# Kernel tuning notes

Hardware: AMD Instinct MI355X
Metric: run time of the kernel (lower is better)

The kernel has to match this reference:

```python
import jax, jax.numpy as jnp
import numpy as np

NUM_GROUPS = 32
EPS = 1e-5


def group_norm(x, scale, bias):
    b, c, h, w = x.shape
    g = NUM_GROUPS
    xg = x.reshape(b, g, c // g, h, w)
    mean = xg.mean(axis=(2, 3, 4), keepdims=True)
    var = xg.var(axis=(2, 3, 4), keepdims=True)
    xn = (xg - mean) * jax.lax.rsqrt(var + EPS)
    xn = xn.reshape(b, c, h, w)
    return xn * scale[None, :, None, None] + bias[None, :, None, None]


def conv1x1(x, w, b):
    # x: [b,c,h,w], w: [o,c], b: [o]
    return jnp.einsum('oc,bchw->bohw', w, x) + b[None, :, None, None]


def setup_inputs() -> dict:
    key = jax.random.key(0)
    ks = jax.random.split(key, 8)
    b, c, h, w = 16, 512, 32, 32
    fan = 1.0 / np.sqrt(c)
    return {
        'x': jax.random.normal(ks[0], (b, c, h, w), dtype=jnp.float32),
        'time_emb': jax.random.normal(ks[1], (b, c), dtype=jnp.float32),
        'y': jax.random.randint(ks[2], (b,), 0, 1000, dtype=jnp.int64),
        'gn_scale': jnp.ones((c,), dtype=jnp.float32),
        'gn_bias': jnp.zeros((c,), dtype=jnp.float32),
        'w_qkv': jax.random.normal(ks[3], (3 * c, c), dtype=jnp.float32) * fan,
        'b_qkv': jax.random.normal(ks[4], (3 * c,), dtype=jnp.float32) * fan,
        'w_out': jax.random.normal(ks[5], (c, c), dtype=jnp.float32) * fan,
        'b_out': jax.random.normal(ks[6], (c,), dtype=jnp.float32) * fan,
    }


def reference(x, time_emb, y, gn_scale, gn_bias, w_qkv, b_qkv, w_out, b_out):
    b, c, h, w = x.shape
    qkv = conv1x1(group_norm(x, gn_scale, gn_bias), w_qkv, b_qkv)  # [b,3c,h,w]
    q, k, v = jnp.split(qkv, 3, axis=1)
    n = h * w
    q = q.transpose(0, 2, 3, 1).reshape(b, n, c)  # [b,n,c]
    k = k.reshape(b, c, n)                        # [b,c,n]
    v = v.transpose(0, 2, 3, 1).reshape(b, n, c)  # [b,n,c]
    scores = jnp.einsum('bnc,bcm->bnm', q, k) * (c ** -0.5)  # [b,n,n]
    attn = jax.nn.softmax(scores, axis=-1)
    out = jnp.einsum('bnm,bmc->bnc', attn, v)     # [b,n,c]
    out = out.reshape(b, h, w, c).transpose(0, 3, 1, 2)
    return conv1x1(out, w_out, b_out) + x
```

## Files before the change

kernel.cpp:

```cpp
#include <hip/hip_runtime.h>
#include <hip/hip_bf16.h>

#define NB   16
#define NC   512
#define NSPA 1024
#define NO3  1536
#define GN_EPS 1e-5f
#define SCL 0.044194173824159216f

typedef __bf16 bf16x8 __attribute__((ext_vector_type(8)));
typedef __bf16 bf16x4 __attribute__((ext_vector_type(4)));
typedef float  f32x4  __attribute__((ext_vector_type(4)));

typedef __attribute__((address_space(3))) void lds_t;
typedef const __attribute__((address_space(1))) void gl_t;
#define GLDS16(g, l) __builtin_amdgcn_global_load_lds((gl_t*)(g), (lds_t*)(l), 16, 0, 0)

__device__ __forceinline__ __bf16 tob(float f) { return (__bf16)f; }

__device__ __forceinline__ int xcd_swz(int cpx) {
  return (blockIdx.x & 7) * cpx + (blockIdx.x >> 3);
}

__global__ void gn_stats_kernel(const float* __restrict__ x,
                                const float* __restrict__ gn_scale,
                                const float* __restrict__ gn_bias,
                                float* __restrict__ coefA,
                                float* __restrict__ coefB) {
  const int L = xcd_swz(64);
  const int b = L >> 5, g = L & 31;
  const float4* base = (const float4*)(x + (size_t)(b * NC + g * 16) * NSPA);
  const int tid = threadIdx.x;
  float s = 0.f, ss = 0.f;
#pragma unroll
  for (int i = 0; i < 16; ++i) {
    float4 v = base[i * 256 + tid];
    s  += (v.x + v.y) + (v.z + v.w);
    ss += (v.x * v.x + v.y * v.y) + (v.z * v.z + v.w * v.w);
  }
#pragma unroll
  for (int off = 32; off; off >>= 1) {
    s  += __shfl_xor(s, off);
    ss += __shfl_xor(ss, off);
  }
  __shared__ float rs[4], rss[4];
  const int wave = tid >> 6, lane = tid & 63;
  if (lane == 0) { rs[wave] = s; rss[wave] = ss; }
  __syncthreads();
  if (tid < 16) {
    float S  = rs[0] + rs[1] + rs[2] + rs[3];
    float SS = rss[0] + rss[1] + rss[2] + rss[3];
    float mean = S * (1.f / 16384.f);
    float var  = SS * (1.f / 16384.f) - mean * mean;
    float rstd = rsqrtf(var + GN_EPS);
    int c = g * 16 + tid;
    float a = gn_scale[c] * rstd;
    coefA[b * NC + c] = a;
    coefB[b * NC + c] = gn_bias[c] - mean * a;
  }
}

__global__ void pack_w_kernel(const float* __restrict__ wq, const float* __restrict__ wo,
                              __bf16* __restrict__ wqb, __bf16* __restrict__ wob) {
  const int t = blockIdx.x * 256 + threadIdx.x;
  const int NQ = NO3 * NC / 4;
  float4 v;
  __bf16* dst;
  if (t < NQ) { v = ((const float4*)wq)[t]; dst = wqb + (size_t)t * 4; }
  else        { v = ((const float4*)wo)[t - NQ]; dst = wob + (size_t)(t - NQ) * 4; }
  bf16x4 w;
  w[0] = tob(v.x); w[1] = tob(v.y); w[2] = tob(v.z); w[3] = tob(v.w);
  *(bf16x4*)dst = w;
}

__global__ void pack_x_kernel(const float* __restrict__ x,
                              const float* __restrict__ coefA,
                              const float* __restrict__ coefB,
                              __bf16* __restrict__ xnT) {
  const int L = xcd_swz(256);
  const int b = L >> 7, rem = L & 127;
  const int c0 = (rem >> 4) * 64, n0 = (rem & 15) * 64;
  __shared__ __bf16 l[64][72];
  const int tid = threadIdx.x;
  const int cl = tid >> 2, seg = (tid & 3) * 16;
  const float ca = coefA[b * NC + c0 + cl], cb = coefB[b * NC + c0 + cl];
  const float4* src = (const float4*)(x + (size_t)(b * NC + c0 + cl) * NSPA + n0 + seg);
#pragma unroll
  for (int i = 0; i < 4; ++i) {
    float4 v = src[i];
    l[seg + i * 4 + 0][cl] = tob(v.x * ca + cb);
    l[seg + i * 4 + 1][cl] = tob(v.y * ca + cb);
    l[seg + i * 4 + 2][cl] = tob(v.z * ca + cb);
    l[seg + i * 4 + 3][cl] = tob(v.w * ca + cb);
  }
  __syncthreads();
#pragma unroll
  for (int i = 0; i < 2; ++i) {
    const int chunk = tid + i * 256;
    const int row = chunk >> 3, s = chunk & 7;
    *(bf16x8*)(xnT + (size_t)(b * NSPA + n0 + row) * NC + c0 + s * 8) =
        *(const bf16x8*)&l[row][s * 8];
  }
}

__device__ __forceinline__ void stage_pair(const __bf16* __restrict__ A, int lda,
                                           const __bf16* __restrict__ B, int ldb,
                                           int k0, __bf16* lAf, __bf16* lBf) {
  const int tid = threadIdx.x;
#pragma unroll
  for (int i = 0; i < 4; ++i) {
    const int idx = tid + i * 256;
    const int srow = idx >> 3;
    const int ss = ((idx & 7) ^ (srow & 7)) * 8;
    GLDS16(A + (size_t)srow * lda + k0 + ss, lAf + idx * 8);
    GLDS16(B + (size_t)srow * ldb + k0 + ss, lBf + idx * 8);
  }
}

__device__ __forceinline__ void gemm_core_db(const __bf16* __restrict__ A, int lda,
                                             const __bf16* __restrict__ B, int ldb,
                                             int K, __bf16 (*lA)[128][64],
                                             __bf16 (*lB)[128][64], f32x4 acc[4][4]) {
  const int tid = threadIdx.x;
  const int lane = tid & 63, wave = tid >> 6;
  const int wm = (wave >> 1) * 64, wn = (wave & 1) * 64;
  const int fr = lane & 15, fg = (lane >> 4) * 8;
  const int nt = K >> 6;

  stage_pair(A, lda, B, ldb, 0, &lA[0][0][0], &lB[0][0][0]);
  asm volatile("s_waitcnt vmcnt(0)" ::: "memory");
  __syncthreads();
  int cur = 0;
  for (int t = 0; t < nt; ++t) {
    if (t + 1 < nt)
      stage_pair(A, lda, B, ldb, (t + 1) * 64, &lA[cur ^ 1][0][0], &lB[cur ^ 1][0][0]);
    __builtin_amdgcn_s_setprio(1);
#pragma unroll
    for (int ks = 0; ks < 2; ++ks) {
      bf16x8 af[4], bfr[4];
#pragma unroll
      for (int mi = 0; mi < 4; ++mi) {
        const int r = wm + mi * 16 + fr;
        af[mi] = *(const bf16x8*)&lA[cur][r][(ks * 32 + fg) ^ ((r & 7) << 3)];
      }
#pragma unroll
      for (int ni = 0; ni < 4; ++ni) {
        const int r = wn + ni * 16 + fr;
        bfr[ni] = *(const bf16x8*)&lB[cur][r][(ks * 32 + fg) ^ ((r & 7) << 3)];
      }
#pragma unroll
      for (int mi = 0; mi < 4; ++mi)
#pragma unroll
        for (int ni = 0; ni < 4; ++ni)
          acc[mi][ni] = __builtin_amdgcn_mfma_f32_16x16x32_bf16(af[mi], bfr[ni], acc[mi][ni], 0, 0, 0);
    }
    __builtin_amdgcn_s_setprio(0);
    if (t + 1 < nt) {
      asm volatile("s_waitcnt vmcnt(0)" ::: "memory");
      __syncthreads();
      cur ^= 1;
    }
  }
}

__global__ __launch_bounds__(256, 2) void qkv_gemm_kernel(
    const __bf16* __restrict__ wqb, const __bf16* __restrict__ xnT,
    const float* __restrict__ bqkv, __bf16* __restrict__ qk, __bf16* __restrict__ v) {
  const int L = xcd_swz(192);
  const int pair = L / 12, mblk = L - pair * 12;
  const int b = pair >> 3;
  const int n0 = (pair & 7) * 128, m0 = mblk * 128;
  __shared__ __bf16 lA[2][128][64], lB[2][128][64];
  f32x4 acc[4][4] = {};
  gemm_core_db(wqb + (size_t)m0 * NC, NC, xnT + ((size_t)b * NSPA + n0) * NC, NC,
               NC, lA, lB, acc);

  const int lane = threadIdx.x & 63, wave = threadIdx.x >> 6;
  const int wm = (wave >> 1) * 64, wn = (wave & 1) * 64;
  const int fr = lane & 15, fq4 = (lane >> 4) * 4;
  if (m0 < NSPA) {
#pragma unroll
    for (int mi = 0; mi < 4; ++mi) {
      const int m = m0 + wm + mi * 16 + fq4;
      const float4 bias = *(const float4*)(bqkv + m);
#pragma unroll
      for (int ni = 0; ni < 4; ++ni) {
        const int n = n0 + wn + ni * 16 + fr;
        bf16x4 w;
        w[0] = tob(acc[mi][ni][0] + bias.x);
        w[1] = tob(acc[mi][ni][1] + bias.y);
        w[2] = tob(acc[mi][ni][2] + bias.z);
        w[3] = tob(acc[mi][ni][3] + bias.w);
        *(bf16x4*)(qk + ((size_t)b * NSPA + n) * NSPA + m) = w;
      }
    }
  } else {
#pragma unroll
    for (int mi = 0; mi < 4; ++mi) {
      const int m = m0 + wm + mi * 16 + fq4;
      const float4 bias = *(const float4*)(bqkv + m);
      const int vr = m - NSPA;
#pragma unroll
      for (int ni = 0; ni < 4; ++ni) {
        const int n = n0 + wn + ni * 16 + fr;
        v[((size_t)b * NC + vr + 0) * NSPA + n] = tob(acc[mi][ni][0] + bias.x);
        v[((size_t)b * NC + vr + 1) * NSPA + n] = tob(acc[mi][ni][1] + bias.y);
        v[((size_t)b * NC + vr + 2) * NSPA + n] = tob(acc[mi][ni][2] + bias.z);
        v[((size_t)b * NC + vr + 3) * NSPA + n] = tob(acc[mi][ni][3] + bias.w);
      }
    }
  }
}

__global__ __launch_bounds__(256, 2) void scores_kernel(const __bf16* __restrict__ qk,
                                                        __bf16* __restrict__ P) {
  const int L = xcd_swz(128);
  const int b = L >> 6, r = L & 63;
  const int i0 = (r >> 3) * 128, j0 = (r & 7) * 128;
  const __bf16* base = qk + (size_t)b * NSPA * NSPA;
  __shared__ __bf16 lA[2][128][64], lB[2][128][64];
  f32x4 acc[4][4] = {};
  gemm_core_db(base + (size_t)j0 * NSPA + NC, NSPA, base + (size_t)i0 * NSPA, NSPA,
               NC, lA, lB, acc);

  const int lane = threadIdx.x & 63, wave = threadIdx.x >> 6;
  const int wm = (wave >> 1) * 64, wn = (wave & 1) * 64;
  const int fr = lane & 15, fq4 = (lane >> 4) * 4;
#pragma unroll
  for (int mi = 0; mi < 4; ++mi) {
    const int j = j0 + wm + mi * 16 + fq4;
#pragma unroll
    for (int ni = 0; ni < 4; ++ni) {
      const int i = i0 + wn + ni * 16 + fr;
      bf16x4 w;
      w[0] = tob(acc[mi][ni][0] * SCL);
      w[1] = tob(acc[mi][ni][1] * SCL);
      w[2] = tob(acc[mi][ni][2] * SCL);
      w[3] = tob(acc[mi][ni][3] * SCL);
      *(bf16x4*)(P + ((size_t)b * NSPA + i) * NSPA + j) = w;
    }
  }
}

__global__ void softmax_kernel(__bf16* __restrict__ P) {
  const int L = xcd_swz(128);
  const int base_row = L * 16 + (threadIdx.x >> 6) * 4;
  const int lane = threadIdx.x & 63;
#pragma unroll
  for (int r = 0; r < 4; ++r) {
    __bf16* p = P + (size_t)(base_row + r) * NSPA + lane * 16;
    bf16x8 v0 = *(const bf16x8*)p;
    bf16x8 v1 = *(const bf16x8*)(p + 8);
    float f[16];
#pragma unroll
    for (int i = 0; i < 8; ++i) { f[i] = (float)v0[i]; f[8 + i] = (float)v1[i]; }
    float m = f[0];
#pragma unroll
    for (int i = 1; i < 16; ++i) m = fmaxf(m, f[i]);
#pragma unroll
    for (int off = 32; off; off >>= 1) m = fmaxf(m, __shfl_xor(m, off));
    float s = 0.f;
#pragma unroll
    for (int i = 0; i < 16; ++i) { f[i] = __expf(f[i] - m); s += f[i]; }
#pragma unroll
    for (int off = 32; off; off >>= 1) s += __shfl_xor(s, off);
    const float inv = 1.f / s;
#pragma unroll
    for (int i = 0; i < 8; ++i) { v0[i] = tob(f[i] * inv); v1[i] = tob(f[8 + i] * inv); }
    *(bf16x8*)p = v0;
    *(bf16x8*)(p + 8) = v1;
  }
}

__global__ __launch_bounds__(256, 2) void pv_kernel(const __bf16* __restrict__ v,
                                                    const __bf16* __restrict__ P,
                                                    __bf16* __restrict__ attn) {
  const int L = xcd_swz(64);
  const int b = L >> 5, r = L & 31;
  const int d0 = (r >> 3) * 128, i0 = (r & 7) * 128;
  __shared__ __bf16 lA[2][128][64], lB[2][128][64];
  f32x4 acc[4][4] = {};
  gemm_core_db(v + ((size_t)b * NC + d0) * NSPA, NSPA,
               P + ((size_t)b * NSPA + i0) * NSPA, NSPA, NSPA, lA, lB, acc);

  const int lane = threadIdx.x & 63, wave = threadIdx.x >> 6;
  const int wm = (wave >> 1) * 64, wn = (wave & 1) * 64;
  const int fr = lane & 15, fq4 = (lane >> 4) * 4;
#pragma unroll
  for (int mi = 0; mi < 4; ++mi) {
    const int d = d0 + wm + mi * 16 + fq4;
#pragma unroll
    for (int ni = 0; ni < 4; ++ni) {
      const int i = i0 + wn + ni * 16 + fr;
      bf16x4 w;
      w[0] = tob(acc[mi][ni][0]);
      w[1] = tob(acc[mi][ni][1]);
      w[2] = tob(acc[mi][ni][2]);
      w[3] = tob(acc[mi][ni][3]);
      *(bf16x4*)(attn + ((size_t)b * NSPA + i) * NC + d) = w;
    }
  }
}

__global__ __launch_bounds__(256, 2) void out_gemm_kernel(
    const __bf16* __restrict__ wob, const __bf16* __restrict__ attn,
    const float* __restrict__ bout, const float* __restrict__ x,
    float* __restrict__ out) {
  const int L = xcd_swz(64);
  const int b = L >> 5, r = L & 31;
  const int m0 = (r >> 3) * 128, n0 = (r & 7) * 128;
  __shared__ __bf16 lA[2][128][64], lB[2][128][64];
  f32x4 acc[4][4] = {};
  gemm_core_db(wob + (size_t)m0 * NC, NC, attn + ((size_t)b * NSPA + n0) * NC, NC,
               NC, lA, lB, acc);

  const int lane = threadIdx.x & 63, wave = threadIdx.x >> 6;
  const int wm = (wave >> 1) * 64, wn = (wave & 1) * 64;
  const int fr = lane & 15, fq4 = (lane >> 4) * 4;
#pragma unroll
  for (int mi = 0; mi < 4; ++mi) {
    const int m = m0 + wm + mi * 16 + fq4;
    const float4 bias = *(const float4*)(bout + m);
#pragma unroll
    for (int ni = 0; ni < 4; ++ni) {
      const int n = n0 + wn + ni * 16 + fr;
      const size_t i0x = ((size_t)b * NC + m) * NSPA + n;
      out[i0x + 0 * NSPA] = acc[mi][ni][0] + bias.x + x[i0x + 0 * NSPA];
      out[i0x + 1 * NSPA] = acc[mi][ni][1] + bias.y + x[i0x + 1 * NSPA];
      out[i0x + 2 * NSPA] = acc[mi][ni][2] + bias.z + x[i0x + 2 * NSPA];
      out[i0x + 3 * NSPA] = acc[mi][ni][3] + bias.w + x[i0x + 3 * NSPA];
    }
  }
}

extern "C" void kernel_launch(void* const* d_in, const int* in_sizes, int n_in,
                              void* d_out, int out_size, void* d_ws, size_t ws_size,
                              hipStream_t stream) {
  const float* x        = (const float*)d_in[0];
  const float* gn_scale = (const float*)d_in[3];
  const float* gn_bias  = (const float*)d_in[4];
  const float* w_qkv    = (const float*)d_in[5];
  const float* b_qkv    = (const float*)d_in[6];
  const float* w_out    = (const float*)d_in[7];
  const float* b_out    = (const float*)d_in[8];
  float* out = (float*)d_out;

  char* ws = (char*)d_ws;
  float*  coefA = (float*)ws;
  float*  coefB = coefA + NB * NC;
  __bf16* xnT   = (__bf16*)(ws + (64 << 10));
  __bf16* attn  = xnT;
  __bf16* wqb   = xnT + (size_t)NB * NSPA * NC;
  __bf16* wob   = wqb + (size_t)NO3 * NC;
  __bf16* vbuf  = wob + (size_t)NC * NC;
  __bf16* P     = vbuf + (size_t)NB * NC * NSPA;
  __bf16* qk    = (__bf16*)d_out;

  gn_stats_kernel<<<dim3(512), 256, 0, stream>>>(x, gn_scale, gn_bias, coefA, coefB);
  pack_w_kernel<<<dim3((NO3 * NC + NC * NC) / 4 / 256), 256, 0, stream>>>(w_qkv, w_out, wqb, wob);
  pack_x_kernel<<<dim3(2048), 256, 0, stream>>>(x, coefA, coefB, xnT);
  qkv_gemm_kernel<<<dim3(1536), 256, 0, stream>>>(wqb, xnT, b_qkv, qk, vbuf);
  scores_kernel<<<dim3(1024), 256, 0, stream>>>(qk, P);
  softmax_kernel<<<dim3(1024), 256, 0, stream>>>(P);
  pv_kernel<<<dim3(512), 256, 0, stream>>>(vbuf, P, attn);
  out_gemm_kernel<<<dim3(512), 256, 0, stream>>>(wob, attn, b_out, x, out);
}
```

Before: 134.4 us.

## Fold Q·K weights and output projection into V via weight-product algebra

Precomputes Wq^T·Wk and Wout·Wv as small weight products so the scores use xn·(M·xn) plus a per-key bias term, and the output projection is folded into V before attention. This removes the separate out-projection GEMM and the Q/K projection GEMMs, replacing the 1536-row QKV projection with a 1024-row one. Softmax-invariant per-query bias terms are dropped and a per-key vector R is added. The cost is extra small kernels, an added bf16 rounding of the combined weights, and a different numerical path.

After: 138.6 us. 3.1% more time.

```diff
diff --git a/kernel.cpp b/kernel.cpp
--- a/kernel.cpp
+++ b/kernel.cpp
@@ -4,7 +4,6 @@
 #define NB   16
 #define NC   512
 #define NSPA 1024
-#define NO3  1536
 #define GN_EPS 1e-5f
 #define SCL 0.044194173824159216f
 
@@ -60,17 +59,155 @@
   }
 }
 
-__global__ void pack_w_kernel(const float* __restrict__ wq, const float* __restrict__ wo,
-                              __bf16* __restrict__ wqb, __bf16* __restrict__ wob) {
-  const int t = blockIdx.x * 256 + threadIdx.x;
-  const int NQ = NO3 * NC / 4;
-  float4 v;
-  __bf16* dst;
-  if (t < NQ) { v = ((const float4*)wq)[t]; dst = wqb + (size_t)t * 4; }
-  else        { v = ((const float4*)wo)[t - NQ]; dst = wob + (size_t)(t - NQ) * 4; }
-  bf16x4 w;
-  w[0] = tob(v.x); w[1] = tob(v.y); w[2] = tob(v.z); w[3] = tob(v.w);
-  *(bf16x4*)dst = w;
+__global__ void transpw_kernel(const float* __restrict__ wq, const float* __restrict__ wo,
+                               __bf16* __restrict__ wqT, __bf16* __restrict__ wkT,
+                               __bf16* __restrict__ wvT, __bf16* __restrict__ wob) {
+  const int id = blockIdx.x;
+  const int tid = threadIdx.x;
+  if (id < 192) {
+    const int mat = id >> 6, tile = id & 63;
+    const int o0 = (tile >> 3) * 64, c0 = (tile & 7) * 64;
+    __bf16* dstT = (mat == 0) ? wqT : (mat == 1) ? wkT : wvT;
+    __shared__ __bf16 l[64][72];
+    const int orr = tid >> 2, seg = (tid & 3) * 16;
+    const float4* src = (const float4*)(wq + (size_t)(mat * NC + o0 + orr) * NC + c0 + seg);
+#pragma unroll
+    for (int i = 0; i < 4; ++i) {
+      float4 v = src[i];
+      l[seg + i * 4 + 0][orr] = tob(v.x);
+      l[seg + i * 4 + 1][orr] = tob(v.y);
+      l[seg + i * 4 + 2][orr] = tob(v.z);
+      l[seg + i * 4 + 3][orr] = tob(v.w);
+    }
+    __syncthreads();
+#pragma unroll
+    for (int i = 0; i < 2; ++i) {
+      const int chunk = tid + i * 256;
+      const int row = chunk >> 3, s = chunk & 7;
+      *(bf16x8*)(dstT + (size_t)(c0 + row) * NC + o0 + s * 8) = *(const bf16x8*)&l[row][s * 8];
+    }
+  } else {
+    const int idx = id - 192;
+#pragma unroll
+    for (int i = 0; i < 4; ++i) {
+      const int t = idx * 1024 + i * 256 + tid;
+      float4 v = ((const float4*)wo)[t];
+      bf16x4 w;
+      w[0] = tob(v.x); w[1] = tob(v.y); w[2] = tob(v.z); w[3] = tob(v.w);
+      *(bf16x4*)(wob + (size_t)t * 4) = w;
+    }
+  }
+}
+
+__device__ __forceinline__ void stage_pair(const __bf16* __restrict__ A, int lda,
+                                           const __bf16* __restrict__ B, int ldb,
+                                           int k0, __bf16* lAf, __bf16* lBf) {
+  const int tid = threadIdx.x;
+#pragma unroll
+  for (int i = 0; i < 4; ++i) {
+    const int idx = tid + i * 256;
+    const int srow = idx >> 3;
+    const int ss = ((idx & 7) ^ (srow & 7)) * 8;
+    GLDS16(A + (size_t)srow * lda + k0 + ss, lAf + idx * 8);
+    GLDS16(B + (size_t)srow * ldb + k0 + ss, lBf + idx * 8);
+  }
+}
+
+__device__ __forceinline__ void gemm_core_db(const __bf16* __restrict__ A, int lda,
+                                             const __bf16* __restrict__ B, int ldb,
+                                             int K, __bf16 (*lA)[128][64],
+                                             __bf16 (*lB)[128][64], f32x4 acc[4][4]) {
+  const int tid = threadIdx.x;
+  const int lane = tid & 63, wave = tid >> 6;
+  const int wm = (wave >> 1) * 64, wn = (wave & 1) * 64;
+  const int fr = lane & 15, fg = (lane >> 4) * 8;
+  const int nt = K >> 6;
+
+  stage_pair(A, lda, B, ldb, 0, &lA[0][0][0], &lB[0][0][0]);
+  asm volatile("s_waitcnt vmcnt(0)" ::: "memory");
+  __syncthreads();
+  int cur = 0;
+  for (int t = 0; t < nt; ++t) {
+    if (t + 1 < nt)
+      stage_pair(A, lda, B, ldb, (t + 1) * 64, &lA[cur ^ 1][0][0], &lB[cur ^ 1][0][0]);
+    __builtin_amdgcn_s_setprio(1);
+#pragma unroll
+    for (int ks = 0; ks < 2; ++ks) {
+      bf16x8 af[4], bfr[4];
+#pragma unroll
+      for (int mi = 0; mi < 4; ++mi) {
+        const int r = wm + mi * 16 + fr;
+        af[mi] = *(const bf16x8*)&lA[cur][r][(ks * 32 + fg) ^ ((r & 7) << 3)];
+      }
+#pragma unroll
+      for (int ni = 0; ni < 4; ++ni) {
+        const int r = wn + ni * 16 + fr;
+        bfr[ni] = *(const bf16x8*)&lB[cur][r][(ks * 32 + fg) ^ ((r & 7) << 3)];
+      }
+#pragma unroll
+      for (int mi = 0; mi < 4; ++mi)
+#pragma unroll
+        for (int ni = 0; ni < 4; ++ni)
+          acc[mi][ni] = __builtin_amdgcn_mfma_f32_16x16x32_bf16(af[mi], bfr[ni], acc[mi][ni], 0, 0, 0);
+    }
+    __builtin_amdgcn_s_setprio(0);
+    if (t + 1 < nt) {
+      asm volatile("s_waitcnt vmcnt(0)" ::: "memory");
+      __syncthreads();
+      cur ^= 1;
+    }
+  }
+}
+
+__global__ __launch_bounds__(256, 2) void smallm_kernel(
+    const __bf16* __restrict__ wqT, const __bf16* __restrict__ wkT,
+    const __bf16* __restrict__ wvT, const __bf16* __restrict__ wob,
+    const float* __restrict__ bqkv, __bf16* __restrict__ Aproj,
+    float* __restrict__ rvec, float* __restrict__ bc) {
+  const int id = blockIdx.x;
+  const bool doM = id < 16;
+  const int sub = doM ? id : id - 16;
+  const int mt = sub >> 2, nt2 = sub & 3;
+  const __bf16* A = doM ? (wqT + (size_t)mt * 128 * NC) : (wob + (size_t)mt * 128 * NC);
+  const __bf16* B = doM ? (wkT + (size_t)nt2 * 128 * NC) : (wvT + (size_t)nt2 * 128 * NC);
+  __shared__ __bf16 lA[2][128][64], lB[2][128][64];
+  f32x4 acc[4][4] = {};
+  gemm_core_db(A, NC, B, NC, NC, lA, lB, acc);
+
+  const int tid = threadIdx.x;
+  const int lane = tid & 63, wave = tid >> 6;
+  const int wm = (wave >> 1) * 64, wn = (wave & 1) * 64;
+  const int fr = lane & 15, fq4 = (lane >> 4) * 4;
+  const int mbase = (doM ? 0 : NC) + mt * 128;
+#pragma unroll
+  for (int mi = 0; mi < 4; ++mi) {
+    const int m = mbase + wm + mi * 16 + fq4;
+#pragma unroll
+    for (int ni = 0; ni < 4; ++ni) {
+      const int n = nt2 * 128 + wn + ni * 16 + fr;
+#pragma unroll
+      for (int r = 0; r < 4; ++r)
+        Aproj[(size_t)(m + r) * NC + n] = tob(acc[mi][ni][r]);
+    }
+  }
+  const bool dodot = doM ? (mt == 0) : (nt2 == 0);
+  if (dodot) {
+    const __bf16* W = doM ? (wkT + (size_t)nt2 * 128 * NC) : (wob + (size_t)mt * 128 * NC);
+    const float* bsrc = doM ? bqkv : (bqkv + 2 * NC);
+    float* dst = (doM ? rvec + nt2 * 128 : bc + mt * 128);
+    const int row = tid >> 1, half = tid & 1;
+    const __bf16* wr = W + (size_t)row * NC + half * 256;
+    const float* br = bsrc + half * 256;
+    float s = 0.f;
+#pragma unroll
+    for (int i = 0; i < 32; ++i) {
+      bf16x8 wv8 = *(const bf16x8*)(wr + i * 8);
+#pragma unroll
+      for (int e = 0; e < 8; ++e) s += (float)wv8[e] * br[i * 8 + e];
+    }
+    s += __shfl_xor(s, 1);
+    if (half == 0) dst[row] = s;
+  }
 }
 
 __global__ void pack_x_kernel(const float* __restrict__ x,
@@ -103,125 +240,83 @@
   }
 }
 
-__device__ __forceinline__ void stage_pair(const __bf16* __restrict__ A, int lda,
-                                           const __bf16* __restrict__ B, int ldb,
-                                           int k0, __bf16* lAf, __bf16* lBf) {
-  const int tid = threadIdx.x;
-#pragma unroll
-  for (int i = 0; i < 4; ++i) {
-    const int idx = tid + i * 256;
-    const int srow = idx >> 3;
-    const int ss = ((idx & 7) ^ (srow & 7)) * 8;
-    GLDS16(A + (size_t)srow * lda + k0 + ss, lAf + idx * 8);
-    GLDS16(B + (size_t)srow * ldb + k0 + ss, lBf + idx * 8);
-  }
-}
-
-__device__ __forceinline__ void gemm_core_db(const __bf16* __restrict__ A, int lda,
-                                             const __bf16* __restrict__ B, int ldb,
-                                             int K, __bf16 (*lA)[128][64],
-                                             __bf16 (*lB)[128][64], f32x4 acc[4][4]) {
-  const int tid = threadIdx.x;
-  const int lane = tid & 63, wave = tid >> 6;
-  const int wm = (wave >> 1) * 64, wn = (wave & 1) * 64;
-  const int fr = lane & 15, fg = (lane >> 4) * 8;
-  const int nt = K >> 6;
-
-  stage_pair(A, lda, B, ldb, 0, &lA[0][0][0], &lB[0][0][0]);
-  asm volatile("s_waitcnt vmcnt(0)" ::: "memory");
-  __syncthreads();
-  int cur = 0;
-  for (int t = 0; t < nt; ++t) {
-    if (t + 1 < nt)
-      stage_pair(A, lda, B, ldb, (t + 1) * 64, &lA[cur ^ 1][0][0], &lB[cur ^ 1][0][0]);
-    __builtin_amdgcn_s_setprio(1);
-#pragma unroll
-    for (int ks = 0; ks < 2; ++ks) {
-      bf16x8 af[4], bfr[4];
-#pragma unroll
-      for (int mi = 0; mi < 4; ++mi) {
-        const int r = wm + mi * 16 + fr;
-        af[mi] = *(const bf16x8*)&lA[cur][r][(ks * 32 + fg) ^ ((r & 7) << 3)];
-      }
-#pragma unroll
-      for (int ni = 0; ni < 4; ++ni) {
-        const int r = wn + ni * 16 + fr;
-        bfr[ni] = *(const bf16x8*)&lB[cur][r][(ks * 32 + fg) ^ ((r & 7) << 3)];
-      }
-#pragma unroll
-      for (int mi = 0; mi < 4; ++mi)
-#pragma unroll
-        for (int ni = 0; ni < 4; ++ni)
-          acc[mi][ni] = __builtin_amdgcn_mfma_f32_16x16x32_bf16(af[mi], bfr[ni], acc[mi][ni], 0, 0, 0);
-    }
-    __builtin_amdgcn_s_setprio(0);
-    if (t + 1 < nt) {
-      asm volatile("s_waitcnt vmcnt(0)" ::: "memory");
-      __syncthreads();
-      cur ^= 1;
-    }
-  }
-}
-
-__global__ __launch_bounds__(256, 2) void qkv_gemm_kernel(
-    const __bf16* __restrict__ wqb, const __bf16* __restrict__ xnT,
-    const float* __restrict__ bqkv, __bf16* __restrict__ qk, __bf16* __restrict__ v) {
-  const int L = xcd_swz(192);
-  const int pair = L / 12, mblk = L - pair * 12;
+__global__ void r_kernel(const __bf16* __restrict__ xnT, const float* __restrict__ rvec,
+                         float* __restrict__ R) {
+  const int L = xcd_swz(32);
+  const int b = L >> 4, j0 = (L & 15) * 64;
+  const int row = threadIdx.x >> 2, q = threadIdx.x & 3;
+  const __bf16* src = xnT + ((size_t)(b * NSPA) + j0 + row) * NC + q * 128;
+  const float* rv = rvec + q * 128;
+  float s = 0.f;
+#pragma unroll
+  for (int i = 0; i < 16; ++i) {
+    bf16x8 v = *(const bf16x8*)(src + i * 8);
+#pragma unroll
+    for (int e = 0; e < 8; ++e) s += (float)v[e] * rv[i * 8 + e];
+  }
+  s += __shfl_xor(s, 1);
+  s += __shfl_xor(s, 2);
+  if (q == 0) R[b * NSPA + j0 + row] = s;
+}
+
+__global__ __launch_bounds__(256, 2) void proj_kernel(
+    const __bf16* __restrict__ Aproj, const __bf16* __restrict__ xnT,
+    const float* __restrict__ bc, __bf16* __restrict__ Yt, __bf16* __restrict__ vp) {
+  const int L = xcd_swz(128);
+  const int pair = L >> 3, mblk = L & 7;
   const int b = pair >> 3;
   const int n0 = (pair & 7) * 128, m0 = mblk * 128;
   __shared__ __bf16 lA[2][128][64], lB[2][128][64];
   f32x4 acc[4][4] = {};
-  gemm_core_db(wqb + (size_t)m0 * NC, NC, xnT + ((size_t)b * NSPA + n0) * NC, NC,
+  gemm_core_db(Aproj + (size_t)m0 * NC, NC, xnT + ((size_t)b * NSPA + n0) * NC, NC,
                NC, lA, lB, acc);
 
   const int lane = threadIdx.x & 63, wave = threadIdx.x >> 6;
   const int wm = (wave >> 1) * 64, wn = (wave & 1) * 64;
   const int fr = lane & 15, fq4 = (lane >> 4) * 4;
-  if (m0 < NSPA) {
+  if (m0 < NC) {
 #pragma unroll
     for (int mi = 0; mi < 4; ++mi) {
       const int m = m0 + wm + mi * 16 + fq4;
-      const float4 bias = *(const float4*)(bqkv + m);
 #pragma unroll
       for (int ni = 0; ni < 4; ++ni) {
         const int n = n0 + wn + ni * 16 + fr;
         bf16x4 w;
-        w[0] = tob(acc[mi][ni][0] + bias.x);
-        w[1] = tob(acc[mi][ni][1] + bias.y);
-        w[2] = tob(acc[mi][ni][2] + bias.z);
-        w[3] = tob(acc[mi][ni][3] + bias.w);
-        *(bf16x4*)(qk + ((size_t)b * NSPA + n) * NSPA + m) = w;
+        w[0] = tob(acc[mi][ni][0]);
+        w[1] = tob(acc[mi][ni][1]);
+        w[2] = tob(acc[mi][ni][2]);
+        w[3] = tob(acc[mi][ni][3]);
+        *(bf16x4*)(Yt + ((size_t)b * NSPA + n) * NC + m) = w;
       }
     }
   } else {
 #pragma unroll
     for (int mi = 0; mi < 4; ++mi) {
       const int m = m0 + wm + mi * 16 + fq4;
-      const float4 bias = *(const float4*)(bqkv + m);
-      const int vr = m - NSPA;
+      const int d = m - NC;
+      const float4 bias = *(const float4*)(bc + d);
 #pragma unroll
       for (int ni = 0; ni < 4; ++ni) {
         const int n = n0 + wn + ni * 16 + fr;
-        v[((size_t)b * NC + vr + 0) * NSPA + n] = tob(acc[mi][ni][0] + bias.x);
-        v[((size_t)b * NC + vr + 1) * NSPA + n] = tob(acc[mi][ni][1] + bias.y);
-        v[((size_t)b * NC + vr + 2) * NSPA + n] = tob(acc[mi][ni][2] + bias.z);
-        v[((size_t)b * NC + vr + 3) * NSPA + n] = tob(acc[mi][ni][3] + bias.w);
+        vp[((size_t)b * NC + d + 0) * NSPA + n] = tob(acc[mi][ni][0] + bias.x);
+        vp[((size_t)b * NC + d + 1) * NSPA + n] = tob(acc[mi][ni][1] + bias.y);
+        vp[((size_t)b * NC + d + 2) * NSPA + n] = tob(acc[mi][ni][2] + bias.z);
+        vp[((size_t)b * NC + d + 3) * NSPA + n] = tob(acc[mi][ni][3] + bias.w);
       }
     }
   }
 }
 
-__global__ __launch_bounds__(256, 2) void scores_kernel(const __bf16* __restrict__ qk,
-                                                        __bf16* __restrict__ P) {
+__global__ __launch_bounds__(256, 2) void scores_kernel(
+    const __bf16* __restrict__ Yt, const __bf16* __restrict__ xnT,
+    const float* __restrict__ R, __bf16* __restrict__ P) {
   const int L = xcd_swz(128);
   const int b = L >> 6, r = L & 63;
   const int i0 = (r >> 3) * 128, j0 = (r & 7) * 128;
-  const __bf16* base = qk + (size_t)b * NSPA * NSPA;
   __shared__ __bf16 lA[2][128][64], lB[2][128][64];
   f32x4 acc[4][4] = {};
-  gemm_core_db(base + (size_t)j0 * NSPA + NC, NSPA, base + (size_t)i0 * NSPA, NSPA,
-               NC, lA, lB, acc);
+  gemm_core_db(Yt + ((size_t)b * NSPA + j0) * NC, NC,
+               xnT + ((size_t)b * NSPA + i0) * NC, NC, NC, lA, lB, acc);
 
   const int lane = threadIdx.x & 63, wave = threadIdx.x >> 6;
   const int wm = (wave >> 1) * 64, wn = (wave & 1) * 64;
@@ -229,14 +324,15 @@
 #pragma unroll
   for (int mi = 0; mi < 4; ++mi) {
     const int j = j0 + wm + mi * 16 + fq4;
+    const float4 Rb = *(const float4*)(R + b * NSPA + j);
 #pragma unroll
     for (int ni = 0; ni < 4; ++ni) {
       const int i = i0 + wn + ni * 16 + fr;
       bf16x4 w;
-      w[0] = tob(acc[mi][ni][0] * SCL);
-      w[1] = tob(acc[mi][ni][1] * SCL);
-      w[2] = tob(acc[mi][ni][2] * SCL);
-      w[3] = tob(acc[mi][ni][3] * SCL);
+      w[0] = tob((acc[mi][ni][0] + Rb.x) * SCL);
+      w[1] = tob((acc[mi][ni][1] + Rb.y) * SCL);
+      w[2] = tob((acc[mi][ni][2] + Rb.z) * SCL);
+      w[3] = tob((acc[mi][ni][3] + Rb.w) * SCL);
       *(bf16x4*)(P + ((size_t)b * NSPA + i) * NSPA + j) = w;
     }
   }
@@ -272,15 +368,16 @@
   }
 }
 
-__global__ __launch_bounds__(256, 2) void pv_kernel(const __bf16* __restrict__ v,
-                                                    const __bf16* __restrict__ P,
-                                                    __bf16* __restrict__ attn) {
+__global__ __launch_bounds__(256, 2) void pvout_kernel(
+    const __bf16* __restrict__ vp, const __bf16* __restrict__ P,
+    const float* __restrict__ bout, const float* __restrict__ x,
+    float* __restrict__ out) {
   const int L = xcd_swz(64);
   const int b = L >> 5, r = L & 31;
   const int d0 = (r >> 3) * 128, i0 = (r & 7) * 128;
   __shared__ __bf16 lA[2][128][64], lB[2][128][64];
   f32x4 acc[4][4] = {};
-  gemm_core_db(v + ((size_t)b * NC + d0) * NSPA, NSPA,
+  gemm_core_db(vp + ((size_t)b * NC + d0) * NSPA, NSPA,
                P + ((size_t)b * NSPA + i0) * NSPA, NSPA, NSPA, lA, lB, acc);
 
   const int lane = threadIdx.x & 63, wave = threadIdx.x >> 6;
@@ -289,46 +386,15 @@
 #pragma unroll
   for (int mi = 0; mi < 4; ++mi) {
     const int d = d0 + wm + mi * 16 + fq4;
+    const float4 bias = *(const float4*)(bout + d);
 #pragma unroll
     for (int ni = 0; ni < 4; ++ni) {
       const int i = i0 + wn + ni * 16 + fr;
-      bf16x4 w;
-      w[0] = tob(acc[mi][ni][0]);
-      w[1] = tob(acc[mi][ni][1]);
-      w[2] = tob(acc[mi][ni][2]);
-      w[3] = tob(acc[mi][ni][3]);
-      *(bf16x4*)(attn + ((size_t)b * NSPA + i) * NC + d) = w;
-    }
-  }
-}
-
-__global__ __launch_bounds__(256, 2) void out_gemm_kernel(
-    const __bf16* __restrict__ wob, const __bf16* __restrict__ attn,
-    const float* __restrict__ bout, const float* __restrict__ x,
-    float* __restrict__ out) {
-  const int L = xcd_swz(64);
-  const int b = L >> 5, r = L & 31;
-  const int m0 = (r >> 3) * 128, n0 = (r & 7) * 128;
-  __shared__ __bf16 lA[2][128][64], lB[2][128][64];
-  f32x4 acc[4][4] = {};
-  gemm_core_db(wob + (size_t)m0 * NC, NC, attn + ((size_t)b * NSPA + n0) * NC, NC,
-               NC, lA, lB, acc);
-
-  const int lane = threadIdx.x & 63, wave = threadIdx.x >> 6;
-  const int wm = (wave >> 1) * 64, wn = (wave & 1) * 64;
-  const int fr = lane & 15, fq4 = (lane >> 4) * 4;
-#pragma unroll
-  for (int mi = 0; mi < 4; ++mi) {
-    const int m = m0 + wm + mi * 16 + fq4;
-    const float4 bias = *(const float4*)(bout + m);
-#pragma unroll
-    for (int ni = 0; ni < 4; ++ni) {
-      const int n = n0 + wn + ni * 16 + fr;
-      const size_t i0x = ((size_t)b * NC + m) * NSPA + n;
-      out[i0x + 0 * NSPA] = acc[mi][ni][0] + bias.x + x[i0x + 0 * NSPA];
-      out[i0x + 1 * NSPA] = acc[mi][ni][1] + bias.y + x[i0x + 1 * NSPA];
-      out[i0x + 2 * NSPA] = acc[mi][ni][2] + bias.z + x[i0x + 2 * NSPA];
-      out[i0x + 3 * NSPA] = acc[mi][ni][3] + bias.w + x[i0x + 3 * NSPA];
+      const size_t ix = ((size_t)b * NC + d) * NSPA + i;
+      out[ix + 0 * NSPA] = acc[mi][ni][0] + bias.x + x[ix + 0 * NSPA];
+      out[ix + 1 * NSPA] = acc[mi][ni][1] + bias.y + x[ix + 1 * NSPA];
+      out[ix + 2 * NSPA] = acc[mi][ni][2] + bias.z + x[ix + 2 * NSPA];
+      out[ix + 3 * NSPA] = acc[mi][ni][3] + bias.w + x[ix + 3 * NSPA];
     }
   }
 }
@@ -345,23 +411,28 @@
   const float* b_out    = (const float*)d_in[8];
   float* out = (float*)d_out;
 
-  char* ws = (char*)d_ws;
-  float*  coefA = (float*)ws;
+  float*  coefA = (float*)d_ws;
   float*  coefB = coefA + NB * NC;
-  __bf16* xnT   = (__bf16*)(ws + (64 << 10));
-  __bf16* attn  = xnT;
-  __bf16* wqb   = xnT + (size_t)NB * NSPA * NC;
-  __bf16* wob   = wqb + (size_t)NO3 * NC;
-  __bf16* vbuf  = wob + (size_t)NC * NC;
-  __bf16* P     = vbuf + (size_t)NB * NC * NSPA;
-  __bf16* qk    = (__bf16*)d_out;
-
+  float*  rvec  = coefB + NB * NC;
+  float*  bc    = rvec + NC;
+  float*  R     = bc + NC;
+  __bf16* wqT   = (__bf16*)(R + NB * NSPA);
+  __bf16* wkT   = wqT + NC * NC;
+  __bf16* wvT   = wkT + NC * NC;
+  __bf16* wob   = wvT + NC * NC;
+  __bf16* Aproj = wob + NC * NC;
+  __bf16* xnT   = Aproj + 2 * NC * NC;
+  __bf16* vp    = xnT + (size_t)NB * NSPA * NC;
+  __bf16* P     = vp + (size_t)NB * NC * NSPA;
+  __bf16* Yt    = (__bf16*)d_out;
+
+  transpw_kernel<<<dim3(256), 256, 0, stream>>>(w_qkv, w_out, wqT, wkT, wvT, wob);
   gn_stats_kernel<<<dim3(512), 256, 0, stream>>>(x, gn_scale, gn_bias, coefA, coefB);
-  pack_w_kernel<<<dim3((NO3 * NC + NC * NC) / 4 / 256), 256, 0, stream>>>(w_qkv, w_out, wqb, wob);
+  smallm_kernel<<<dim3(32), 256, 0, stream>>>(wqT, wkT, wvT, wob, b_qkv, Aproj, rvec, bc);
   pack_x_kernel<<<dim3(2048), 256, 0, stream>>>(x, coefA, coefB, xnT);
-  qkv_gemm_kernel<<<dim3(1536), 256, 0, stream>>>(wqb, xnT, b_qkv, qk, vbuf);
-  scores_kernel<<<dim3(1024), 256, 0, stream>>>(qk, P);
+  r_kernel<<<dim3(256), 256, 0, stream>>>(xnT, rvec, R);
+  proj_kernel<<<dim3(1024), 256, 0, stream>>>(Aproj, xnT, bc, Yt, vp);
+  scores_kernel<<<dim3(1024), 256, 0, stream>>>(Yt, xnT, R, P);
   softmax_kernel<<<dim3(1024), 256, 0, stream>>>(P);
-  pv_kernel<<<dim3(512), 256, 0, stream>>>(vbuf, P, attn);
-  out_gemm_kernel<<<dim3(512), 256, 0, stream>>>(wob, attn, b_out, x, out);
-}
+  pvout_kernel<<<dim3(512), 256, 0, stream>>>(vp, P, b_out, x, out);
+}
```
